# Kernel optimization log

Measured on AMD Instinct MI355X. Metric: run time of the kernel, lower is better.

## Reference

```python
import jax, jax.numpy as jnp
import numpy as np

B, N, D = 4096, 32768, 1024

def _l2norm(x, eps=1e-12):
    # matches F.normalize(p=2, dim=-1): x / max(||x||, eps)
    n = jnp.sqrt(jnp.sum(x * x, axis=-1, keepdims=True))
    return x / jnp.maximum(n, eps)

def setup_inputs() -> dict:
    key = jax.random.key(0)
    k1, k2, k3 = jax.random.split(key, 3)
    return {
        "query": jax.random.normal(k1, (B, D), dtype=jnp.float32),
        "keys": jax.random.normal(k2, (N, D), dtype=jnp.float32),
        "values": jax.random.normal(k3, (N, D), dtype=jnp.float32),
    }

def reference(query, keys, values):
    q = _l2norm(query.astype(jnp.float32))          # [B, D]
    k = _l2norm(keys.astype(jnp.float32))           # [N, D]
    v = values.astype(jnp.float32)                  # [N, Dv]
    sim = jnp.einsum('bd,nd->bn', q, k)             # [B, N] cosine similarities
    # torch .var(dim=-1) is unbiased (ddof=1)
    attention_var = jnp.var(sim, axis=-1, ddof=1).mean()
    best = jnp.argmax(sim, axis=-1)                 # [B]
    retrieved = v[best]                             # [B, Dv] gather
    return retrieved, attention_var
```

## Files before the change

kernel.cpp:

```cpp
#include <hip/hip_runtime.h>
#include <math.h>
#include <stdint.h>

#define B_ 4096
#define N_ 32768
#define D_ 1024

#define BM 128
#define BN 128
#define NT 2
#define NCHUNK 128
#define KTOT 32
#define QG (B_ / 16)
#define KG (N_ / 16)

typedef __attribute__((ext_vector_type(8))) short short8;
typedef __attribute__((ext_vector_type(4))) float f4;
typedef unsigned short u16;

__device__ __forceinline__ u16 bf16_rn(float x) {
    uint32_t u = __float_as_uint(x);
    u += 0x7fffu + ((u >> 16) & 1u);
    return (u16)(u >> 16);
}

__device__ __forceinline__ void split4(f4 v, uint2& hpack, uint2& lpack) {
    u16 h[4], l[4];
    #pragma unroll
    for (int e = 0; e < 4; ++e) {
        float x = v[e];
        u16 hb = bf16_rn(x);
        float hf = __uint_as_float(((uint32_t)hb) << 16);
        h[e] = hb;
        l[e] = bf16_rn(x - hf);
    }
    hpack.x = (uint32_t)h[0] | ((uint32_t)h[1] << 16);
    hpack.y = (uint32_t)h[2] | ((uint32_t)h[3] << 16);
    lpack.x = (uint32_t)l[0] | ((uint32_t)l[1] << 16);
    lpack.y = (uint32_t)l[2] | ((uint32_t)l[3] << 16);
}

__device__ __forceinline__ void g2l16(const void* g, void* l) {
    __builtin_amdgcn_global_load_lds(
        (const __attribute__((address_space(1))) char*)(uintptr_t)g,
        (__attribute__((address_space(3))) char*)(uint32_t)(uintptr_t)l,
        16, 0, 0);
}

__global__ __launch_bounds__(256) void pack_kernel(
    const float* __restrict__ q, const float* __restrict__ k,
    float* __restrict__ invq, float* __restrict__ invk,
    u16* __restrict__ qhi, u16* __restrict__ qlo,
    u16* __restrict__ khi, u16* __restrict__ klo,
    float* __restrict__ out)
{
    const int g = blockIdx.x;
    const int lane = threadIdx.x & 63;
    const int w = threadIdx.x >> 6;

    const float* src; float* invdst;
    u16 *dhi, *dlo; int groups, gg;
    if (g < B_ / 16) { src = q; invdst = invq; dhi = qhi; dlo = qlo; groups = QG; gg = g; }
    else { src = k; invdst = invk; dhi = khi; dlo = klo; groups = KG; gg = g - B_ / 16; }

    const int row = gg * 16 + (lane & 15);
    const int kofs = (lane >> 4) * 8;
    const float* rp = src + (size_t)row * D_;

    f4 v0[8], v1[8];
    float s = 0.f;
    #pragma unroll
    for (int u = 0; u < 8; ++u) {
        const int kt = w + u * 4;
        v0[u] = *(const f4*)(rp + kt * 32 + kofs);
        v1[u] = *(const f4*)(rp + kt * 32 + kofs + 4);
        #pragma unroll
        for (int e = 0; e < 4; ++e) {
            s = fmaf(v0[u][e], v0[u][e], s);
            s = fmaf(v1[u][e], v1[u][e], s);
        }
    }
    s += __shfl_xor(s, 16);
    s += __shfl_xor(s, 32);
    __shared__ float red[4][16];
    if ((lane >> 4) == 0) red[w][lane & 15] = s;
    __syncthreads();
    const float tot = red[0][lane & 15] + red[1][lane & 15]
                    + red[2][lane & 15] + red[3][lane & 15];
    const float scale = 1.0f / fmaxf(sqrtf(tot), 1e-12f);
    if (w == 0 && lane < 16) invdst[gg * 16 + lane] = scale;

    #pragma unroll
    for (int u = 0; u < 8; ++u) {
        const int kt = w + u * 4;
        f4 a = v0[u] * scale, b = v1[u] * scale;
        uint2 h0, l0, h1, l1;
        split4(a, h0, l0);
        split4(b, h1, l1);
        const size_t cbase = ((size_t)kt * groups + gg) * 512 + lane * 8;
        uint4 hh = {h0.x, h0.y, h1.x, h1.y};
        uint4 ll = {l0.x, l0.y, l1.x, l1.y};
        *(uint4*)(dhi + cbase) = hh;
        *(uint4*)(dlo + cbase) = ll;
    }
    if (g == 0 && threadIdx.x == 0) out[(size_t)B_ * D_] = 0.0f;
}

__global__ __launch_bounds__(256, 4) void sim_stats_kernel(
    const u16* __restrict__ qhi, const u16* __restrict__ qlo,
    const u16* __restrict__ khi, const u16* __restrict__ klo,
    float* __restrict__ partials)
{
    __shared__ __align__(16) char smem[34816];

    const int tid = threadIdx.x;
    const int lane = tid & 63;
    const int w = tid >> 6;
    const int wm = w >> 1, wn = w & 1;
    const int quad = lane >> 4;
    const int l16 = lane & 15;
    const int mtile = blockIdx.x;
    const int chunk = blockIdx.y;
    const int b0 = mtile * BM;

    const int aG0 = (b0 >> 4) + wm * 4;
    const int plane = w >> 1;
    const u16* __restrict__ kbase = plane ? klo : khi;
    const int sub0 = (w & 1) * 4;
    char* const dst0 = smem + plane * 8192 + sub0 * 1024;

    float (*scan)[68] = (float(*)[68])smem;

    float r_sum = 0.f, r_sq = 0.f, r_m1 = -INFINITY, r_m2 = -INFINITY;
    int r_i1 = 0x7fffffff, r_i2 = 0x7fffffff;

    const f4 zf = {0.f, 0.f, 0.f, 0.f};

    for (int nt = 0; nt < NT; ++nt) {
        const int n0 = chunk * (BN * NT) + nt * BN;
        const int g0 = n0 >> 4;

        __syncthreads();
        {
            const size_t cb = ((size_t)(g0 + sub0)) * 512 + lane * 8;
            #pragma unroll
            for (int t = 0; t < 4; ++t)
                g2l16(kbase + cb + t * 512, dst0 + t * 1024);
        }

        f4 acc[4][4];
        #pragma unroll
        for (int i = 0; i < 4; ++i)
            #pragma unroll
            for (int j = 0; j < 4; ++j) acc[i][j] = zf;

        for (int kt = 0; kt < KTOT; ++kt) {
            const int cur = kt & 1;
            __syncthreads();

            short8 ah[4], al[4];
            {
                const size_t ab = ((size_t)kt * QG + aG0) * 512 + lane * 8;
                #pragma unroll
                for (int i = 0; i < 4; ++i) {
                    ah[i] = *(const short8*)(qhi + ab + i * 512);
                    al[i] = *(const short8*)(qlo + ab + i * 512);
                }
            }

            if (kt + 1 < KTOT) {
                const size_t cb = ((size_t)(kt + 1) * KG + g0 + sub0) * 512 + lane * 8;
                char* dst = smem + (1 - cur) * 16384 + plane * 8192 + sub0 * 1024;
                #pragma unroll
                for (int t = 0; t < 4; ++t)
                    g2l16(kbase + cb + t * 512, dst + t * 1024);
            }

            const char* cbuf = smem + cur * 16384;
            #pragma unroll
            for (int j = 0; j < 4; ++j) {
                short8 bh = *(const short8*)(cbuf + (wn * 4 + j) * 1024 + lane * 16);
                short8 bl = *(const short8*)(cbuf + 8192 + (wn * 4 + j) * 1024 + lane * 16);
                #pragma unroll
                for (int i = 0; i < 4; ++i) {
                    acc[i][j] = __builtin_amdgcn_mfma_f32_16x16x32_bf16(ah[i], bh, acc[i][j], 0, 0, 0);
                    acc[i][j] = __builtin_amdgcn_mfma_f32_16x16x32_bf16(ah[i], bl, acc[i][j], 0, 0, 0);
                    acc[i][j] = __builtin_amdgcn_mfma_f32_16x16x32_bf16(al[i], bh, acc[i][j], 0, 0, 0);
                }
            }
        }

        const int srow = tid >> 1;
        const int c0 = (tid & 1) * 32;
        #pragma unroll 1
        for (int h = 0; h < 2; ++h) {
            __syncthreads();
            if (wn == h) {
                #pragma unroll
                for (int i = 0; i < 4; ++i)
                    #pragma unroll
                    for (int j = 0; j < 4; ++j)
                        #pragma unroll
                        for (int p = 0; p < 4; ++p)
                            scan[wm*64 + i*16 + quad*4 + p][j*16 + l16] = acc[i][j][p];
            }
            __syncthreads();
            const int gbase = n0 + h * 64 + c0;
            #pragma unroll
            for (int u = 0; u < 8; ++u) {
                const f4 v = *(const f4*)&scan[srow][c0 + 4*u];
                #pragma unroll
                for (int e = 0; e < 4; ++e) {
                    const float sv = v[e];
                    const int gi = gbase + 4*u + e;
                    r_sum += sv;
                    r_sq = fmaf(sv, sv, r_sq);
                    if (sv > r_m1)      { r_m2 = r_m1; r_i2 = r_i1; r_m1 = sv; r_i1 = gi; }
                    else if (sv > r_m2) { r_m2 = sv; r_i2 = gi; }
                }
            }
        }
    }

    __syncthreads();
    float* mb = (float*)smem;
    mb[tid*6+0] = r_sum; mb[tid*6+1] = r_sq;
    mb[tid*6+2] = r_m1;  mb[tid*6+3] = __int_as_float(r_i1);
    mb[tid*6+4] = r_m2;  mb[tid*6+5] = __int_as_float(r_i2);
    __syncthreads();
    if ((tid & 1) == 0) {
        const float* o = mb + (size_t)(tid + 1) * 6;
        const float bs = o[0], bq = o[1], bm1 = o[2], bm2 = o[4];
        const int bi1 = __float_as_int(o[3]), bi2 = __float_as_int(o[5]);
        float s = r_sum + bs, q2 = r_sq + bq;
        float m1 = r_m1, m2 = r_m2; int i1 = r_i1, i2 = r_i2;
        if (bm1 > m1 || (bm1 == m1 && bi1 < i1)) {
            float nm2; int ni2;
            if (m1 > bm2 || (m1 == bm2 && i1 < bi2)) { nm2 = m1; ni2 = i1; }
            else                                     { nm2 = bm2; ni2 = bi2; }
            m1 = bm1; i1 = bi1; m2 = nm2; i2 = ni2;
        } else if (bm1 > m2 || (bm1 == m2 && bi1 < i2)) {
            m2 = bm1; i2 = bi1;
        }
        const int row = b0 + (tid >> 1);
        float* p = partials + ((size_t)row * NCHUNK + chunk) * 8;
        f4 p0 = {s, q2, m1, __int_as_float(i1)};
        f4 p1 = {m2, __int_as_float(i2), 0.f, 0.f};
        *(f4*)p = p0;
        *(f4*)(p + 4) = p1;
    }
}

__global__ __launch_bounds__(64) void finalize_kernel(
    const float* __restrict__ partials,
    const float* __restrict__ qg, const float* __restrict__ kg,
    const float* __restrict__ values,
    const float* __restrict__ invq, const float* __restrict__ invk,
    float* __restrict__ out)
{
    const int b = blockIdx.x;
    const int lane = threadIdx.x;

    float s = 0.f, q2 = 0.f, m1 = -INFINITY, m2 = -INFINITY;
    int i1 = 0x7fffffff, i2 = 0x7fffffff;
    #pragma unroll
    for (int cc = 0; cc < NCHUNK / 64; ++cc) {
        const int c = lane + cc * 64;
        const float* p = partials + ((size_t)b * NCHUNK + c) * 8;
        const float bs = p[0], bq = p[1], bm1 = p[2], bm2 = p[4];
        const int bi1 = __float_as_int(p[3]), bi2 = __float_as_int(p[5]);
        s += bs; q2 += bq;
        if (bm1 > m1 || (bm1 == m1 && bi1 < i1)) {
            float nm2; int ni2;
            if (m1 > bm2 || (m1 == bm2 && i1 < bi2)) { nm2 = m1; ni2 = i1; }
            else                                     { nm2 = bm2; ni2 = bi2; }
            m1 = bm1; i1 = bi1; m2 = nm2; i2 = ni2;
        } else if (bm1 > m2 || (bm1 == m2 && bi1 < i2)) {
            m2 = bm1; i2 = bi1;
        }
    }
    #pragma unroll
    for (int msk = 1; msk < 64; msk <<= 1) {
        const float bs = __shfl_xor(s, msk), bq = __shfl_xor(q2, msk);
        const float bm1 = __shfl_xor(m1, msk), bm2 = __shfl_xor(m2, msk);
        const int bi1 = __shfl_xor(i1, msk), bi2 = __shfl_xor(i2, msk);
        s += bs; q2 += bq;
        if (bm1 > m1 || (bm1 == m1 && bi1 < i1)) {
            float nm2; int ni2;
            if (m1 > bm2 || (m1 == bm2 && i1 < bi2)) { nm2 = m1; ni2 = i1; }
            else                                     { nm2 = bm2; ni2 = bi2; }
            m1 = bm1; i1 = bi1; m2 = nm2; i2 = ni2;
        } else if (bm1 > m2 || (bm1 == m2 && bi1 < i2)) {
            m2 = bm1; i2 = bi1;
        }
    }
    if (lane == 0) {
        const float var = (q2 - s * s / (float)N_) / (float)(N_ - 1);
        atomicAdd(out + (size_t)B_ * D_, var * (1.0f / B_));
    }

    const float* qrow = qg + (size_t)b * D_;
    const float* k1 = kg + (size_t)i1 * D_;
    const float* k2 = kg + (size_t)i2 * D_;
    double d1 = 0.0, d2 = 0.0;
    #pragma unroll
    for (int v4 = 0; v4 < 4; ++v4) {
        const int off = v4 * 256 + lane * 4;
        const f4 qv = *(const f4*)(qrow + off);
        const f4 a1 = *(const f4*)(k1 + off);
        const f4 a2 = *(const f4*)(k2 + off);
        #pragma unroll
        for (int e = 0; e < 4; ++e) {
            d1 += (double)qv[e] * (double)a1[e];
            d2 += (double)qv[e] * (double)a2[e];
        }
    }
    #pragma unroll
    for (int msk = 1; msk < 64; msk <<= 1) {
        d1 += __shfl_xor(d1, msk);
        d2 += __shfl_xor(d2, msk);
    }
    const double sc = (double)invq[b];
    const double s1 = d1 * sc * (double)invk[i1];
    const double s2 = d2 * sc * (double)invk[i2];
    const int winner = (s2 > s1 || (s2 == s1 && i2 < i1)) ? i2 : i1;

    const float* vrow = values + (size_t)winner * D_;
    float* orow = out + (size_t)b * D_;
    #pragma unroll
    for (int v4 = 0; v4 < 4; ++v4) {
        const int off = v4 * 256 + lane * 4;
        *(f4*)(orow + off) = *(const f4*)(vrow + off);
    }
}

extern "C" void kernel_launch(void* const* d_in, const int* in_sizes, int n_in,
                              void* d_out, int out_size, void* d_ws, size_t ws_size,
                              hipStream_t stream)
{
    const float* q = (const float*)d_in[0];
    const float* k = (const float*)d_in[1];
    const float* v = (const float*)d_in[2];
    float* out = (float*)d_out;
    float* ws = (float*)d_ws;

    float* invq = ws;
    float* invk = ws + B_;
    float* partials = ws + B_ + N_;
    u16* qhi = (u16*)(partials + (size_t)B_ * NCHUNK * 8);
    u16* qlo = qhi + (size_t)B_ * D_;
    u16* khi = qlo + (size_t)B_ * D_;
    u16* klo = khi + (size_t)N_ * D_;

    pack_kernel<<<(B_ + N_) / 16, 256, 0, stream>>>(q, k, invq, invk, qhi, qlo, khi, klo, out);
    sim_stats_kernel<<<dim3(B_ / BM, NCHUNK), 256, 0, stream>>>(qhi, qlo, khi, klo, partials);
    finalize_kernel<<<B_, 64, 0, stream>>>(partials, q, k, v, invq, invk, out);
}
```

Measured before the change: 1.020 ms.

## Stage query tiles through LDS alongside key tiles instead of direct global loads

The A operand (query hi/lo split) is now copied into shared memory with the same double-buffered async global-to-LDS path as the keys, each wave loading one of four planes. Previously each wave read its query fragments straight from global memory every k-step. Shared memory grows from 34 KB to 64 KB per block and the occupancy hint of 4 blocks is dropped, which lowers the number of resident blocks per CU.

Measured after the change: 980.2 us. 3.9% less time.

```diff
diff --git a/kernel.cpp b/kernel.cpp
--- a/kernel.cpp
+++ b/kernel.cpp
@@ -106,12 +106,12 @@
     if (g == 0 && threadIdx.x == 0) out[(size_t)B_ * D_] = 0.0f;
 }
 
-__global__ __launch_bounds__(256, 4) void sim_stats_kernel(
+__global__ __launch_bounds__(256) void sim_stats_kernel(
     const u16* __restrict__ qhi, const u16* __restrict__ qlo,
     const u16* __restrict__ khi, const u16* __restrict__ klo,
     float* __restrict__ partials)
 {
-    __shared__ __align__(16) char smem[34816];
+    __shared__ __align__(16) char smem[65536];
 
     const int tid = threadIdx.x;
     const int lane = tid & 63;
@@ -123,11 +123,8 @@
     const int chunk = blockIdx.y;
     const int b0 = mtile * BM;
 
-    const int aG0 = (b0 >> 4) + wm * 4;
-    const int plane = w >> 1;
-    const u16* __restrict__ kbase = plane ? klo : khi;
-    const int sub0 = (w & 1) * 4;
-    char* const dst0 = smem + plane * 8192 + sub0 * 1024;
+    const u16* sbase = (w == 0) ? qhi : (w == 1) ? qlo : (w == 2) ? khi : klo;
+    const int groups = (w < 2) ? (B_ / 16) : (N_ / 16);
 
     float (*scan)[68] = (float(*)[68])smem;
 
@@ -138,14 +135,15 @@
 
     for (int nt = 0; nt < NT; ++nt) {
         const int n0 = chunk * (BN * NT) + nt * BN;
-        const int g0 = n0 >> 4;
+        const int g0 = ((w < 2) ? b0 : n0) >> 4;
 
         __syncthreads();
         {
-            const size_t cb = ((size_t)(g0 + sub0)) * 512 + lane * 8;
-            #pragma unroll
-            for (int t = 0; t < 4; ++t)
-                g2l16(kbase + cb + t * 512, dst0 + t * 1024);
+            const size_t cb = ((size_t)0 * groups + g0) * 512 + lane * 8;
+            char* dst = smem + w * 8192;
+            #pragma unroll
+            for (int t = 0; t < 8; ++t)
+                g2l16(sbase + cb + t * 512, dst + t * 1024);
         }
 
         f4 acc[4][4];
@@ -157,30 +155,25 @@
         for (int kt = 0; kt < KTOT; ++kt) {
             const int cur = kt & 1;
             __syncthreads();
+            if (kt + 1 < KTOT) {
+                const size_t cb = ((size_t)(kt + 1) * groups + g0) * 512 + lane * 8;
+                char* dst = smem + (1 - cur) * 32768 + w * 8192;
+                #pragma unroll
+                for (int t = 0; t < 8; ++t)
+                    g2l16(sbase + cb + t * 512, dst + t * 1024);
+            }
+            const char* cbuf = smem + cur * 32768;
 
             short8 ah[4], al[4];
-            {
-                const size_t ab = ((size_t)kt * QG + aG0) * 512 + lane * 8;
-                #pragma unroll
-                for (int i = 0; i < 4; ++i) {
-                    ah[i] = *(const short8*)(qhi + ab + i * 512);
-                    al[i] = *(const short8*)(qlo + ab + i * 512);
-                }
-            }
-
-            if (kt + 1 < KTOT) {
-                const size_t cb = ((size_t)(kt + 1) * KG + g0 + sub0) * 512 + lane * 8;
-                char* dst = smem + (1 - cur) * 16384 + plane * 8192 + sub0 * 1024;
-                #pragma unroll
-                for (int t = 0; t < 4; ++t)
-                    g2l16(kbase + cb + t * 512, dst + t * 1024);
-            }
-
-            const char* cbuf = smem + cur * 16384;
+            #pragma unroll
+            for (int i = 0; i < 4; ++i) {
+                ah[i] = *(const short8*)(cbuf + (wm * 4 + i) * 1024 + lane * 16);
+                al[i] = *(const short8*)(cbuf + 8192 + (wm * 4 + i) * 1024 + lane * 16);
+            }
             #pragma unroll
             for (int j = 0; j < 4; ++j) {
-                short8 bh = *(const short8*)(cbuf + (wn * 4 + j) * 1024 + lane * 16);
-                short8 bl = *(const short8*)(cbuf + 8192 + (wn * 4 + j) * 1024 + lane * 16);
+                short8 bh = *(const short8*)(cbuf + 16384 + (wn * 4 + j) * 1024 + lane * 16);
+                short8 bl = *(const short8*)(cbuf + 24576 + (wn * 4 + j) * 1024 + lane * 16);
                 #pragma unroll
                 for (int i = 0; i < 4; ++i) {
                     acc[i][j] = __builtin_amdgcn_mfma_f32_16x16x32_bf16(ah[i], bh, acc[i][j], 0, 0, 0);
```

## Stage query tiles in LDS and pipeline hi/lo planes across phases

Applied to the files above, without the earlier changes.

The query hi/lo fragments are no longer read straight from global memory by every wave. Both query and key tiles are now staged through LDS, with the hi plane in one buffer and the lo plane in another. Each k-step is split into two phases: the hi×hi products run while the lo planes load, then the lo products run while the next hi planes load. This cuts redundant global query reads, in exchange for an extra barrier per k-step and a lower occupancy hint of 3 instead of 4.

After: 935.3 us. 1.09x faster.

```diff
diff --git a/kernel.cpp b/kernel.cpp
--- a/kernel.cpp
+++ b/kernel.cpp
@@ -106,7 +106,7 @@
     if (g == 0 && threadIdx.x == 0) out[(size_t)B_ * D_] = 0.0f;
 }
 
-__global__ __launch_bounds__(256, 4) void sim_stats_kernel(
+__global__ __launch_bounds__(256, 3) void sim_stats_kernel(
     const u16* __restrict__ qhi, const u16* __restrict__ qlo,
     const u16* __restrict__ khi, const u16* __restrict__ klo,
     float* __restrict__ partials)
@@ -123,11 +123,15 @@
     const int chunk = blockIdx.y;
     const int b0 = mtile * BM;
 
-    const int aG0 = (b0 >> 4) + wm * 4;
-    const int plane = w >> 1;
-    const u16* __restrict__ kbase = plane ? klo : khi;
-    const int sub0 = (w & 1) * 4;
-    char* const dst0 = smem + plane * 8192 + sub0 * 1024;
+    const u16* p1base = (w < 2) ? qhi : khi;
+    const u16* p2base = (w < 2) ? qlo : klo;
+    const int grpw = (w < 2) ? QG : KG;
+    const int aG0 = b0 >> 4;
+
+    char* const buf0 = smem;
+    char* const buf1 = smem + 16384;
+    char* const dstw0 = buf0 + w * 4096;
+    char* const dstw1 = buf1 + w * 4096;
 
     float (*scan)[68] = (float(*)[68])smem;
 
@@ -138,14 +142,14 @@
 
     for (int nt = 0; nt < NT; ++nt) {
         const int n0 = chunk * (BN * NT) + nt * BN;
-        const int g0 = n0 >> 4;
+        const int gw0 = ((w < 2) ? aG0 : (n0 >> 4)) + (w & 1) * 4;
 
         __syncthreads();
         {
-            const size_t cb = ((size_t)(g0 + sub0)) * 512 + lane * 8;
+            const size_t cb = ((size_t)gw0) * 512 + lane * 8;
             #pragma unroll
             for (int t = 0; t < 4; ++t)
-                g2l16(kbase + cb + t * 512, dst0 + t * 1024);
+                g2l16(p1base + cb + t * 512, dstw0 + t * 1024);
         }
 
         f4 acc[4][4];
@@ -155,38 +159,45 @@
             for (int j = 0; j < 4; ++j) acc[i][j] = zf;
 
         for (int kt = 0; kt < KTOT; ++kt) {
-            const int cur = kt & 1;
             __syncthreads();
-
-            short8 ah[4], al[4];
             {
-                const size_t ab = ((size_t)kt * QG + aG0) * 512 + lane * 8;
-                #pragma unroll
-                for (int i = 0; i < 4; ++i) {
-                    ah[i] = *(const short8*)(qhi + ab + i * 512);
-                    al[i] = *(const short8*)(qlo + ab + i * 512);
-                }
-            }
-
+                const size_t cb = ((size_t)kt * grpw + gw0) * 512 + lane * 8;
+                #pragma unroll
+                for (int t = 0; t < 4; ++t)
+                    g2l16(p2base + cb + t * 512, dstw1 + t * 1024);
+            }
+            short8 ah[4], bh[4];
+            #pragma unroll
+            for (int i = 0; i < 4; ++i) {
+                ah[i] = *(const short8*)(buf0 + (wm * 4 + i) * 1024 + lane * 16);
+                bh[i] = *(const short8*)(buf0 + 8192 + (wn * 4 + i) * 1024 + lane * 16);
+            }
+            #pragma unroll
+            for (int j = 0; j < 4; ++j)
+                #pragma unroll
+                for (int i = 0; i < 4; ++i)
+                    acc[i][j] = __builtin_amdgcn_mfma_f32_16x16x32_bf16(ah[i], bh[j], acc[i][j], 0, 0, 0);
+
+            __syncthreads();
             if (kt + 1 < KTOT) {
-                const size_t cb = ((size_t)(kt + 1) * KG + g0 + sub0) * 512 + lane * 8;
-                char* dst = smem + (1 - cur) * 16384 + plane * 8192 + sub0 * 1024;
+                const size_t cb = ((size_t)(kt + 1) * grpw + gw0) * 512 + lane * 8;
                 #pragma unroll
                 for (int t = 0; t < 4; ++t)
-                    g2l16(kbase + cb + t * 512, dst + t * 1024);
-            }
-
-            const char* cbuf = smem + cur * 16384;
+                    g2l16(p1base + cb + t * 512, dstw0 + t * 1024);
+            }
             #pragma unroll
             for (int j = 0; j < 4; ++j) {
-                short8 bh = *(const short8*)(cbuf + (wn * 4 + j) * 1024 + lane * 16);
-                short8 bl = *(const short8*)(cbuf + 8192 + (wn * 4 + j) * 1024 + lane * 16);
-                #pragma unroll
-                for (int i = 0; i < 4; ++i) {
-                    acc[i][j] = __builtin_amdgcn_mfma_f32_16x16x32_bf16(ah[i], bh, acc[i][j], 0, 0, 0);
+                const short8 bl = *(const short8*)(buf1 + 8192 + (wn * 4 + j) * 1024 + lane * 16);
+                #pragma unroll
+                for (int i = 0; i < 4; ++i)
                     acc[i][j] = __builtin_amdgcn_mfma_f32_16x16x32_bf16(ah[i], bl, acc[i][j], 0, 0, 0);
-                    acc[i][j] = __builtin_amdgcn_mfma_f32_16x16x32_bf16(al[i], bh, acc[i][j], 0, 0, 0);
-                }
+            }
+            #pragma unroll
+            for (int i = 0; i < 4; ++i) {
+                const short8 al = *(const short8*)(buf1 + (wm * 4 + i) * 1024 + lane * 16);
+                #pragma unroll
+                for (int j = 0; j < 4; ++j)
+                    acc[i][j] = __builtin_amdgcn_mfma_f32_16x16x32_bf16(al, bh[j], acc[i][j], 0, 0, 0);
             }
         }
 
```
